# Kernel optimization log

Hardware: AMD Instinct MI355X
Metric: run time of the kernel (lower is better)

## Reference

```python
import jax, jax.numpy as jnp
import numpy as np

HIDDEN = 2048
NH = 32        # query heads
NKV = 4        # kv heads (GQA)
HD = 64        # head_dim
Q_SIZE = NH * HD      # 2048
KV_SIZE = NKV * HD    # 256
WINDOW = 1024         # sliding window size
THETA = 1000000.0
T = 2048              # tokens
SCALE = HD ** -0.5
NEG = -1e30


def setup_inputs() -> dict:
    key = jax.random.key(0)
    k1, k2, k3 = jax.random.split(key, 3)
    return {
        "positions": jnp.arange(T, dtype=jnp.int32),
        "hidden_states": jax.random.normal(k1, (T, HIDDEN), dtype=jnp.float32),
        "wqkv": jax.random.normal(k2, (HIDDEN, Q_SIZE + 2 * KV_SIZE), dtype=jnp.float32) * (HIDDEN ** -0.5),
        "wo": jax.random.normal(k3, (Q_SIZE, HIDDEN), dtype=jnp.float32) * (Q_SIZE ** -0.5),
    }


def _apply_rope(x, positions):
    # NeoX-style rotary embedding over full head_dim (rotate halves).
    half = HD // 2
    inv_freq = 1.0 / (THETA ** (jnp.arange(half, dtype=jnp.float32) / half))
    ang = positions.astype(jnp.float32)[:, None] * inv_freq[None, :]   # [T, half]
    cos = jnp.cos(ang)[:, None, :]   # [T, 1, half]
    sin = jnp.sin(ang)[:, None, :]
    x1, x2 = jnp.split(x, 2, axis=-1)
    return jnp.concatenate([x1 * cos - x2 * sin, x2 * cos + x1 * sin], axis=-1)


def reference(positions, hidden_states, wqkv, wo):
    # fused QKV projection
    qkv = hidden_states @ wqkv                          # [T, Q+2KV]
    q = qkv[:, :Q_SIZE].reshape(T, NH, HD)
    k = qkv[:, Q_SIZE:Q_SIZE + KV_SIZE].reshape(T, NKV, HD)
    v = qkv[:, Q_SIZE + KV_SIZE:].reshape(T, NKV, HD)
    # rotary embedding on q, k
    q = _apply_rope(q, positions)
    k = _apply_rope(k, positions)
    # GQA: repeat kv heads to match query heads
    group = NH // NKV
    kr = jnp.repeat(k, group, axis=1)                   # [T, NH, HD]
    vr = jnp.repeat(v, group, axis=1)
    scores = jnp.einsum('qhd,khd->hqk', q, kr) * SCALE  # [NH, T, T]
    # causal + sliding-window mask: attend to j in (i-WINDOW, i]
    i = jnp.arange(T)[:, None]
    j = jnp.arange(T)[None, :]
    mask = (j <= i) & (i - j < WINDOW)                  # [T, T]
    scores = jnp.where(mask[None, :, :], scores, NEG)
    probs = jax.nn.softmax(scores, axis=-1)
    attn = jnp.einsum('hqk,khd->qhd', probs, vr).reshape(T, Q_SIZE)
    return attn @ wo                                    # [T, HIDDEN]
```

## Files before the change

kernel.cpp:

```cpp
#include <hip/hip_runtime.h>
#include <hip/hip_bf16.h>

typedef float  f32x4  __attribute__((ext_vector_type(4)));
typedef __bf16 bf16x8 __attribute__((ext_vector_type(8)));
typedef __bf16 bf16x4 __attribute__((ext_vector_type(4)));
typedef __bf16 bf16x2 __attribute__((ext_vector_type(2)));

#define T_SEQ   2048
#define HIDDEN  2048
#define NH      32
#define NKV     4
#define HD      64
#define QSZ     2048
#define KVSZ    256
#define QKVN    2560
#define WINDOW  1024

#if __has_builtin(__builtin_amdgcn_exp2f)
#define EXPS(x) __builtin_amdgcn_exp2f(x)
#define QSCALE  0.1803368801111f
#else
#define EXPS(x) __expf(x)
#define QSCALE  0.125f
#endif

#define RAW_BARRIER()   asm volatile("s_barrier" ::: "memory")
#define WAITV(n)        asm volatile("s_waitcnt vmcnt(" #n ")" ::: "memory")

__device__ __forceinline__ void gll16(const __bf16* g, __bf16* l) {
    __builtin_amdgcn_global_load_lds(
        (const __attribute__((address_space(1))) void*)g,
        (__attribute__((address_space(3))) void*)l,
        16, 0, 0);
}

__global__ __launch_bounds__(256) void prep(const float4* __restrict__ hidden4,
                                            bf16x4* __restrict__ hidden_bf4,
                                            const float* __restrict__ wqkv,
                                            __bf16* __restrict__ wqkv_t,
                                            const int* __restrict__ pos,
                                            float2* __restrict__ ropetab) {
    __shared__ float tile[32][132];
    const int b = blockIdx.x;
    const int tid = threadIdx.x;

    if (b < 4096) {
        int id = b * 256 + tid;
        float4 v = hidden4[id];
        bf16x4 o;
        o[0] = (__bf16)v.x; o[1] = (__bf16)v.y; o[2] = (__bf16)v.z; o[3] = (__bf16)v.w;
        hidden_bf4[id] = o;
        return;
    }
    if (b < 4352) {
        int id = (b - 4096) * 256 + tid;
        int row = id >> 5, f = id & 31;
        float p = (float)pos[row];
        float ifr = exp2f((float)f * -0.62286151779138f);
        float sn, cs;
        sincosf(p * ifr, &sn, &cs);
        ropetab[id] = make_float2(cs, sn);
        return;
    }

    int t = b - 4352;
    const int bx = t % 20, by = t / 20;
    const int ri = by * 32, ci = bx * 128;
    const int r0 = tid >> 5;
    const int c4 = tid & 31;
    #pragma unroll
    for (int i = 0; i < 4; i++) {
        float4 v = *reinterpret_cast<const float4*>(
            &wqkv[(size_t)(ri + r0 + i * 8) * QKVN + ci + c4 * 4]);
        *reinterpret_cast<float4*>(&tile[r0 + i * 8][c4 * 4]) = v;
    }
    __syncthreads();
    const int c  = tid >> 3;
    const int rb = tid & 7;
    #pragma unroll
    for (int j = 0; j < 4; j++) {
        int cc = c + j * 32;
        bf16x4 pk;
        #pragma unroll
        for (int i = 0; i < 4; i++) pk[i] = (__bf16)tile[rb * 4 + i][cc];
        *reinterpret_cast<bf16x4*>(&wqkv_t[(size_t)(ci + cc) * HIDDEN + ri + rb * 4]) = pk;
    }
}


#define GEMM_PROLOGUE_COMMON(Aptr, Btptr, Kdim)                                 \
    const int tid = threadIdx.x;                                                \
    const int wid = tid >> 6;                                                   \
    const int l   = tid & 63;                                                   \
    const int lg  = l >> 4;                                                     \
    const int ll  = l & 15;                                                     \
    const int swl = ll & 7;                                                     \
    const int wm  = wid >> 1, wn = wid & 1;                                     \
    const int gx   = gridDim.x;                                                 \
    const int flat = blockIdx.y * gx + blockIdx.x;                              \
    const int nwg  = gx * gridDim.y;                                            \
    const int swz  = (flat & 7) * (nwg >> 3) + (flat >> 3);                     \
    const int bm   = (swz / gx) * 64;                                           \
    const int bn   = (swz % gx) * 128;                                          \
    const __bf16* Ab = (Aptr) + (size_t)bm * (Kdim);                            \
    const __bf16* Bb = (Btptr) + (size_t)bn * (Kdim);                           \
    f32x4 acc[2][4];                                                            \
    _Pragma("unroll")                                                           \
    for (int i = 0; i < 2; i++)                                                 \
        _Pragma("unroll")                                                       \
        for (int j = 0; j < 4; j++)                                             \
            acc[i][j] = (f32x4){0.f, 0.f, 0.f, 0.f};                            \
    const int srow = tid >> 3;                                                  \
    const int sseg0 = tid & 7;

#define GEMM_STAGE(buf, k0, Kdim)                                               \
    {                                                                           \
        _Pragma("unroll")                                                       \
        for (int c = 0; c < 2; c++) {                                           \
            int row  = c * 32 + srow;                                           \
            int sseg = sseg0 ^ (row & 7);                                       \
            gll16(Ab + (size_t)row * (Kdim) + (k0) + sseg * 8,                  \
                  &Asm[buf][(c * 256 + tid) * 8]);                              \
        }                                                                       \
        _Pragma("unroll")                                                       \
        for (int c = 0; c < 4; c++) {                                           \
            int row  = c * 32 + srow;                                           \
            int sseg = sseg0 ^ (row & 7);                                       \
            gll16(Bb + (size_t)row * (Kdim) + (k0) + sseg * 8,                  \
                  &Bsm[buf][(c * 256 + tid) * 8]);                              \
        }                                                                       \
    }

#define GEMM_COMPUTE(bufidx)                                                    \
    _Pragma("unroll")                                                           \
    for (int ss = 0; ss < 2; ss++) {                                            \
        bf16x8 af[2], bfr[4];                                                   \
        _Pragma("unroll")                                                       \
        for (int mi = 0; mi < 2; mi++) {                                        \
            int r = wm * 32 + mi * 16 + ll;                                     \
            int u = (ss * 4 + lg) ^ swl;                                        \
            af[mi] = *reinterpret_cast<const bf16x8*>(&Asm[bufidx][r * 64 + u * 8]); \
        }                                                                       \
        _Pragma("unroll")                                                       \
        for (int ni = 0; ni < 4; ni++) {                                        \
            int r = wn * 64 + ni * 16 + ll;                                     \
            int u = (ss * 4 + lg) ^ swl;                                        \
            bfr[ni] = *reinterpret_cast<const bf16x8*>(&Bsm[bufidx][r * 64 + u * 8]); \
        }                                                                       \
        _Pragma("unroll")                                                       \
        for (int mi = 0; mi < 2; mi++)                                          \
            _Pragma("unroll")                                                   \
            for (int ni = 0; ni < 4; ni++)                                      \
                acc[mi][ni] = __builtin_amdgcn_mfma_f32_16x16x32_bf16(          \
                    af[mi], bfr[ni], acc[mi][ni], 0, 0, 0);                     \
    }

#define GEMM_KLOOP2(Kdim)                                                       \
    GEMM_STAGE(0, 0, Kdim)                                                      \
    int cur = 0;                                                                \
    for (int k0 = 0; k0 < (Kdim); k0 += 64) {                                   \
        RAW_BARRIER();                                                          \
        if (k0 + 64 < (Kdim)) {                                                 \
            GEMM_STAGE(cur ^ 1, k0 + 64, Kdim)                                  \
            WAITV(6);                                                           \
        } else {                                                                \
            WAITV(0);                                                           \
        }                                                                       \
        RAW_BARRIER();                                                          \
        __builtin_amdgcn_sched_barrier(0);                                      \
        GEMM_COMPUTE(cur)                                                       \
        cur ^= 1;                                                               \
    }

#define GEMM_KLOOP3(Kdim)                                                       \
    GEMM_STAGE(0, 0, Kdim)                                                      \
    GEMM_STAGE(1, 64, Kdim)                                                     \
    int cur = 0;                                                                \
    for (int k0 = 0; k0 < (Kdim); k0 += 64) {                                   \
        if (k0 + 64 < (Kdim)) { WAITV(6); } else { WAITV(0); }                  \
        RAW_BARRIER();                                                          \
        __builtin_amdgcn_sched_barrier(0);                                      \
        if (k0 + 128 < (Kdim)) {                                                \
            int nb = cur + 2; if (nb >= 3) nb -= 3;                             \
            GEMM_STAGE(nb, k0 + 128, Kdim)                                      \
        }                                                                       \
        GEMM_COMPUTE(cur)                                                       \
        cur = (cur == 2) ? 0 : cur + 1;                                         \
    }

__global__ __launch_bounds__(256) void gemm_out(const __bf16* __restrict__ A,
                                                const __bf16* __restrict__ Bt,
                                                float* __restrict__ Cout,
                                                int M, int N, int K) {
    __shared__ __align__(16) __bf16 Asm[3][64 * 64];
    __shared__ __align__(16) __bf16 Bsm[3][128 * 64];
    GEMM_PROLOGUE_COMMON(A, Bt, K)
    GEMM_KLOOP3(K)
    #pragma unroll
    for (int mi = 0; mi < 2; mi++)
        #pragma unroll
        for (int ni = 0; ni < 4; ni++)
            #pragma unroll
            for (int r = 0; r < 4; r++) {
                int row = bm + wm*32 + mi*16 + lg*4 + r;
                int col = bn + wn*64 + ni*16 + ll;
                Cout[(size_t)row * N + col] = acc[mi][ni][r];
            }
}

__global__ __launch_bounds__(256) void gemm_qkv(const __bf16* __restrict__ A,
                                                const __bf16* __restrict__ Bt,
                                                const float2* __restrict__ ropetab,
                                                __bf16* __restrict__ q,
                                                __bf16* __restrict__ k,
                                                __bf16* __restrict__ vT) {
    __shared__ __align__(16) __bf16 Asm[2][64 * 64];
    __shared__ __align__(16) __bf16 Bsm[2][128 * 64];
    GEMM_PROLOGUE_COMMON(A, Bt, HIDDEN)
    GEMM_KLOOP2(HIDDEN)

    if (bn < QSZ + KVSZ) {
        const bool isq = (bn < QSZ);
        #pragma unroll
        for (int mi = 0; mi < 2; mi++) {
            #pragma unroll
            for (int r = 0; r < 4; r++) {
                int row = bm + wm*32 + mi*16 + lg*4 + r;
                const float2* tb = &ropetab[row * 32 + ll];
                #pragma unroll
                for (int ni = 0; ni < 2; ni++) {
                    float2 cssn = tb[ni * 16];
                    float x1 = acc[mi][ni][r], x2 = acc[mi][ni + 2][r];
                    float o1 = x1 * cssn.x - x2 * cssn.y;
                    float o2 = x2 * cssn.x + x1 * cssn.y;
                    int col = bn + wn*64 + ni*16 + ll;
                    if (isq) {
                        q[(size_t)row * QSZ + col]      = (__bf16)(o1 * QSCALE);
                        q[(size_t)row * QSZ + col + 32] = (__bf16)(o2 * QSCALE);
                    } else {
                        k[(size_t)row * KVSZ + (col - QSZ)]      = (__bf16)o1;
                        k[(size_t)row * KVSZ + (col - QSZ) + 32] = (__bf16)o2;
                    }
                }
            }
        }
    } else {
        #pragma unroll
        for (int mi = 0; mi < 2; mi++) {
            int row0 = bm + wm*32 + mi*16 + lg*4;
            #pragma unroll
            for (int ni = 0; ni < 4; ni++) {
                int d = bn + wn*64 + ni*16 + ll - (QSZ + KVSZ);
                bf16x4 pk;
                #pragma unroll
                for (int r = 0; r < 4; r++) pk[r] = (__bf16)acc[mi][ni][r];
                *reinterpret_cast<bf16x4*>(&vT[(size_t)d * T_SEQ + row0]) = pk;
            }
        }
    }
}

__global__ __launch_bounds__(512) void attn_fused(const __bf16* __restrict__ qg,
                                                  const __bf16* __restrict__ kgl,
                                                  const __bf16* __restrict__ vTg,
                                                  __bf16* __restrict__ og,
                                                  const float* __restrict__ wo,
                                                  __bf16* __restrict__ wo_t) {
    __shared__ __align__(16) char smem[49152];
    const int b   = blockIdx.x;
    const int tid = threadIdx.x;

    if (b >= 512) {
        float (*tile)[132] = (float(*)[132])smem;
        int t = b - 512;
        const int bx = t & 15, by = t >> 4;
        const int ri = by * 32, ci = bx * 128;
        const int r0 = tid >> 4;
        const int c8 = tid & 15;
        #pragma unroll
        for (int j = 0; j < 2; j++) {
            int col = c8 * 8 + j * 4;
            float4 v = *reinterpret_cast<const float4*>(
                &wo[(size_t)(ri + r0) * HIDDEN + ci + col]);
            *reinterpret_cast<float4*>(&tile[r0][col]) = v;
        }
        __syncthreads();
        #pragma unroll
        for (int j = 0; j < 2; j++) {
            int u  = tid + j * 512;
            int cc = u >> 3;
            int rb = u & 7;
            bf16x4 pk;
            #pragma unroll
            for (int i = 0; i < 4; i++) pk[i] = (__bf16)tile[rb * 4 + i][cc];
            *reinterpret_cast<bf16x4*>(&wo_t[(size_t)(ci + cc) * HIDDEN + ri + rb * 4]) = pk;
        }
        return;
    }

    __bf16* Ksm = (__bf16*)smem;
    __bf16* VTs = (__bf16*)(smem + 24576);
#define KSM(buf) (Ksm + (buf) * 4096)
#define VSM(buf) (VTs + (buf) * 4096)

    const int qb  = b & 31;
    const int hp  = b >> 5;
    const int kvh = hp >> 2;
    const int wid = tid >> 6;
    const int h   = hp * 2 + (wid >> 2);
    const int l   = tid & 63;
    const int lg  = l >> 4;
    const int ll  = l & 15;
    const int i0  = qb * 64;
    const int qw  = i0 + (wid & 3) * 16;
    const int qi  = qw + ll;

    bf16x8 qf[2];
    {
        const __bf16* qp = qg + (size_t)(qw + ll) * QSZ + h * 64 + lg * 8;
        qf[0] = *reinterpret_cast<const bf16x8*>(qp);
        qf[1] = *reinterpret_cast<const bf16x8*>(qp + 32);
    }

    f32x4 o[4];
    #pragma unroll
    for (int dn = 0; dn < 4; dn++) o[dn] = (f32x4){0.f, 0.f, 0.f, 0.f};
    float l_run = 0.f;

    int jlo = i0 - (WINDOW - 1); if (jlo < 0) jlo = 0;
    int t0v = jlo & ~63;
    int tend = i0 + 64;

    const int srow = tid >> 3;
    const int sg   = (tid & 7) ^ (srow & 7);
    const int krow = (srow & 35) | ((srow & 8) << 1) | ((srow & 4) << 1) | ((srow & 16) >> 2);
    const __bf16* kp = kgl + (size_t)krow * KVSZ + kvh * 64 + sg * 8;
    const __bf16* vp = vTg + (size_t)(kvh * 64 + srow) * T_SEQ + sg * 8;

#define ASTAGE(buf, t)                                   \
    {                                                    \
        gll16(kp + (size_t)(t) * KVSZ, KSM(buf) + tid * 8); \
        gll16(vp + (t),                VSM(buf) + tid * 8); \
    }

    ASTAGE(0, t0v);
    if (t0v + 64 < tend) ASTAGE(1, t0v + 64);

    const int swl = ll & 7;
    const int u0 = (lg ^ swl) * 8;
    const int u1 = ((4 + lg) ^ swl) * 8;

    int cur = 0;
    for (int t = t0v; t < tend; t += 64) {
        if (t + 64 < tend) { WAITV(2); } else { WAITV(0); }
        RAW_BARRIER();
        __builtin_amdgcn_sched_barrier(0);
        if (t + 128 < tend) {
            int nb = cur + 2; if (nb >= 3) nb -= 3;
            ASTAGE(nb, t + 128);
        }

        bool active = (t <= qw + 15) && (t + 63 >= qw - (WINDOW - 1));
        if (active) {
            f32x4 sT[4];
            __builtin_amdgcn_s_setprio(1);
            #pragma unroll
            for (int kt = 0; kt < 4; kt++) {
                sT[kt] = (f32x4){0.f, 0.f, 0.f, 0.f};
                bf16x8 kf0 = *reinterpret_cast<const bf16x8*>(KSM(cur) + kt*1024 + ll*64 + u0);
                sT[kt] = __builtin_amdgcn_mfma_f32_16x16x32_bf16(kf0, qf[0], sT[kt], 0, 0, 0);
                bf16x8 kf1 = *reinterpret_cast<const bf16x8*>(KSM(cur) + kt*1024 + ll*64 + u1);
                sT[kt] = __builtin_amdgcn_mfma_f32_16x16x32_bf16(kf1, qf[1], sT[kt], 0, 0, 0);
            }
            __builtin_amdgcn_s_setprio(0);

            bool full = (t + 63 <= qw) && (t >= qw + 15 - (WINDOW - 1));
            float ts = 0.f;
            if (full) {
                #pragma unroll
                for (int kt = 0; kt < 4; kt++) {
                    #pragma unroll
                    for (int r = 0; r < 4; r++) {
                        float p = EXPS(sT[kt][r]);
                        sT[kt][r] = p;
                        ts += p;
                    }
                }
            } else {
                #pragma unroll
                for (int kt = 0; kt < 4; kt++) {
                    int jb = t + ((kt & 2) << 4) + ((kt & 1) << 2) + (lg << 3);
                    #pragma unroll
                    for (int r = 0; r < 4; r++) {
                        int j = jb + r;
                        bool ok = (j <= qi) && (qi - j < WINDOW);
                        float p = ok ? EXPS(sT[kt][r]) : 0.f;
                        sT[kt][r] = p;
                        ts += p;
                    }
                }
            }
            ts += __shfl_xor(ts, 16);
            ts += __shfl_xor(ts, 32);
            l_run += ts;

            __builtin_amdgcn_s_setprio(1);
            #pragma unroll
            for (int kt2 = 0; kt2 < 2; kt2++) {
                bf16x8 pa;
                #pragma unroll
                for (int r = 0; r < 4; r++) {
                    pa[r]     = (__bf16)sT[kt2*2][r];
                    pa[r + 4] = (__bf16)sT[kt2*2 + 1][r];
                }
                int uv = kt2 ? u1 : u0;
                #pragma unroll
                for (int dn = 0; dn < 4; dn++) {
                    bf16x8 vf = *reinterpret_cast<const bf16x8*>(VSM(cur) + dn*1024 + ll*64 + uv);
                    o[dn] = __builtin_amdgcn_mfma_f32_16x16x32_bf16(pa, vf, o[dn], 0, 0, 0);
                }
            }
            __builtin_amdgcn_s_setprio(0);
        }
        cur = (cur == 2) ? 0 : cur + 1;
    }
#undef ASTAGE
#undef KSM
#undef VSM

    float linv = 1.0f / l_run;
    float i0v = __shfl(linv, lg*4 + 0);
    float i1v = __shfl(linv, lg*4 + 1);
    float i2v = __shfl(linv, lg*4 + 2);
    float i3v = __shfl(linv, lg*4 + 3);
    #pragma unroll
    for (int dn = 0; dn < 4; dn++) {
        og[(size_t)(qw + lg*4 + 0) * QSZ + h*64 + dn*16 + ll] = (__bf16)(o[dn][0] * i0v);
        og[(size_t)(qw + lg*4 + 1) * QSZ + h*64 + dn*16 + ll] = (__bf16)(o[dn][1] * i1v);
        og[(size_t)(qw + lg*4 + 2) * QSZ + h*64 + dn*16 + ll] = (__bf16)(o[dn][2] * i2v);
        og[(size_t)(qw + lg*4 + 3) * QSZ + h*64 + dn*16 + ll] = (__bf16)(o[dn][3] * i3v);
    }
}

extern "C" void kernel_launch(void* const* d_in, const int* in_sizes, int n_in,
                              void* d_out, int out_size, void* d_ws, size_t ws_size,
                              hipStream_t stream) {
    const int*   positions = (const int*)d_in[0];
    const float* hidden    = (const float*)d_in[1];
    const float* wqkv      = (const float*)d_in[2];
    const float* wo        = (const float*)d_in[3];
    float* out = (float*)d_out;

    char* ws = (char*)d_ws;
    __bf16* hidden_bf = (__bf16*)(ws);
    __bf16* wqkv_t    = (__bf16*)(ws + 8388608);
    __bf16* wo_t      = (__bf16*)(ws + 18874368);
    __bf16* q_bf      = (__bf16*)(ws + 37748736);
    __bf16* k_bf      = (__bf16*)(ws + 46137344);
    __bf16* vT_bf     = (__bf16*)(ws + 47185920);
    __bf16* attn_bf   = (__bf16*)(ws + 48234496);
    float2* ropetab   = (float2*)(ws + 56623104);

    prep<<<dim3(5632), dim3(256), 0, stream>>>(
        (const float4*)hidden, (bf16x4*)hidden_bf, wqkv, wqkv_t, positions, ropetab);

    gemm_qkv<<<dim3(QKVN / 128, T_SEQ / 64), dim3(256), 0, stream>>>(
        hidden_bf, wqkv_t, ropetab, q_bf, k_bf, vT_bf);

    attn_fused<<<dim3(1536), dim3(512), 0, stream>>>(
        q_bf, k_bf, vT_bf, attn_bf, wo, wo_t);

    gemm_out<<<dim3(HIDDEN / 128, T_SEQ / 64), dim3(256), 0, stream>>>(
        attn_bf, wo_t, out, T_SEQ, HIDDEN, QSZ);
}
```

Baseline: 102.0 us.

## Fuse fp32-to-bf16 hidden conversion into QKV GEMM A-tile loading

Removes the separate conversion pass that wrote a bf16 copy of hidden_states in prep. The QKV GEMM now loads fp32 A tiles into registers, converts them to bf16, and writes them to LDS, while B tiles still use direct global-to-LDS loads. This saves one full read and write of the activations plus a slice of the prep launch. In exchange, the GEMM reads twice the A bytes from global memory on every tile and now waits on register loads before the LDS writes, which may expose latency in the double-buffered loop.

```diff
diff --git a/kernel.cpp b/kernel.cpp
--- a/kernel.cpp
+++ b/kernel.cpp
@@ -26,6 +26,7 @@
 
 #define RAW_BARRIER()   asm volatile("s_barrier" ::: "memory")
 #define WAITV(n)        asm volatile("s_waitcnt vmcnt(" #n ")" ::: "memory")
+#define WAITLGKM0()     asm volatile("s_waitcnt lgkmcnt(0)" ::: "memory")
 
 __device__ __forceinline__ void gll16(const __bf16* g, __bf16* l) {
     __builtin_amdgcn_global_load_lds(
@@ -34,9 +35,7 @@
         16, 0, 0);
 }
 
-__global__ __launch_bounds__(256) void prep(const float4* __restrict__ hidden4,
-                                            bf16x4* __restrict__ hidden_bf4,
-                                            const float* __restrict__ wqkv,
+__global__ __launch_bounds__(256) void prep(const float* __restrict__ wqkv,
                                             __bf16* __restrict__ wqkv_t,
                                             const int* __restrict__ pos,
                                             float2* __restrict__ ropetab) {
@@ -44,16 +43,8 @@
     const int b = blockIdx.x;
     const int tid = threadIdx.x;
 
-    if (b < 4096) {
+    if (b < 256) {
         int id = b * 256 + tid;
-        float4 v = hidden4[id];
-        bf16x4 o;
-        o[0] = (__bf16)v.x; o[1] = (__bf16)v.y; o[2] = (__bf16)v.z; o[3] = (__bf16)v.w;
-        hidden_bf4[id] = o;
-        return;
-    }
-    if (b < 4352) {
-        int id = (b - 4096) * 256 + tid;
         int row = id >> 5, f = id & 31;
         float p = (float)pos[row];
         float ifr = exp2f((float)f * -0.62286151779138f);
@@ -63,7 +54,7 @@
         return;
     }
 
-    int t = b - 4352;
+    int t = b - 256;
     const int bx = t % 20, by = t / 20;
     const int ri = by * 32, ci = bx * 128;
     const int r0 = tid >> 5;
@@ -88,7 +79,7 @@
 }
 
 
-#define GEMM_PROLOGUE_COMMON(Aptr, Btptr, Kdim)                                 \
+#define GEMM_IDX_COMMON()                                                       \
     const int tid = threadIdx.x;                                                \
     const int wid = tid >> 6;                                                   \
     const int l   = tid & 63;                                                   \
@@ -102,8 +93,6 @@
     const int swz  = (flat & 7) * (nwg >> 3) + (flat >> 3);                     \
     const int bm   = (swz / gx) * 64;                                           \
     const int bn   = (swz % gx) * 128;                                          \
-    const __bf16* Ab = (Aptr) + (size_t)bm * (Kdim);                            \
-    const __bf16* Bb = (Btptr) + (size_t)bn * (Kdim);                           \
     f32x4 acc[2][4];                                                            \
     _Pragma("unroll")                                                           \
     for (int i = 0; i < 2; i++)                                                 \
@@ -155,23 +144,6 @@
                     af[mi], bfr[ni], acc[mi][ni], 0, 0, 0);                     \
     }
 
-#define GEMM_KLOOP2(Kdim)                                                       \
-    GEMM_STAGE(0, 0, Kdim)                                                      \
-    int cur = 0;                                                                \
-    for (int k0 = 0; k0 < (Kdim); k0 += 64) {                                   \
-        RAW_BARRIER();                                                          \
-        if (k0 + 64 < (Kdim)) {                                                 \
-            GEMM_STAGE(cur ^ 1, k0 + 64, Kdim)                                  \
-            WAITV(6);                                                           \
-        } else {                                                                \
-            WAITV(0);                                                           \
-        }                                                                       \
-        RAW_BARRIER();                                                          \
-        __builtin_amdgcn_sched_barrier(0);                                      \
-        GEMM_COMPUTE(cur)                                                       \
-        cur ^= 1;                                                               \
-    }
-
 #define GEMM_KLOOP3(Kdim)                                                       \
     GEMM_STAGE(0, 0, Kdim)                                                      \
     GEMM_STAGE(1, 64, Kdim)                                                     \
@@ -194,7 +166,9 @@
                                                 int M, int N, int K) {
     __shared__ __align__(16) __bf16 Asm[3][64 * 64];
     __shared__ __align__(16) __bf16 Bsm[3][128 * 64];
-    GEMM_PROLOGUE_COMMON(A, Bt, K)
+    GEMM_IDX_COMMON()
+    const __bf16* Ab = A  + (size_t)bm * K;
+    const __bf16* Bb = Bt + (size_t)bn * K;
     GEMM_KLOOP3(K)
     #pragma unroll
     for (int mi = 0; mi < 2; mi++)
@@ -208,7 +182,7 @@
             }
 }
 
-__global__ __launch_bounds__(256) void gemm_qkv(const __bf16* __restrict__ A,
+__global__ __launch_bounds__(256) void gemm_qkv(const float* __restrict__ Af,
                                                 const __bf16* __restrict__ Bt,
                                                 const float2* __restrict__ ropetab,
                                                 __bf16* __restrict__ q,
@@ -216,8 +190,68 @@
                                                 __bf16* __restrict__ vT) {
     __shared__ __align__(16) __bf16 Asm[2][64 * 64];
     __shared__ __align__(16) __bf16 Bsm[2][128 * 64];
-    GEMM_PROLOGUE_COMMON(A, Bt, HIDDEN)
-    GEMM_KLOOP2(HIDDEN)
+    GEMM_IDX_COMMON()
+    const float*  Ab = Af + (size_t)bm * HIDDEN;
+    const __bf16* Bb = Bt + (size_t)bn * HIDDEN;
+
+#define QKV_A_LOAD(k0)                                                          \
+    _Pragma("unroll")                                                           \
+    for (int c = 0; c < 2; c++) {                                               \
+        int row  = c * 32 + srow;                                               \
+        int useg = sseg0 ^ (row & 7);                                           \
+        const float4* src = reinterpret_cast<const float4*>(                    \
+            Ab + (size_t)row * HIDDEN + (k0) + useg * 8);                       \
+        fa[c][0] = src[0];                                                      \
+        fa[c][1] = src[1];                                                      \
+    }
+
+#define QKV_A_WRITE(buf)                                                        \
+    _Pragma("unroll")                                                           \
+    for (int c = 0; c < 2; c++) {                                               \
+        bf16x8 w;                                                               \
+        w[0] = (__bf16)fa[c][0].x; w[1] = (__bf16)fa[c][0].y;                   \
+        w[2] = (__bf16)fa[c][0].z; w[3] = (__bf16)fa[c][0].w;                   \
+        w[4] = (__bf16)fa[c][1].x; w[5] = (__bf16)fa[c][1].y;                   \
+        w[6] = (__bf16)fa[c][1].z; w[7] = (__bf16)fa[c][1].w;                   \
+        *reinterpret_cast<bf16x8*>(&Asm[buf][(c * 256 + tid) * 8]) = w;         \
+    }
+
+#define QKV_B_STAGE(buf, k0)                                                    \
+    _Pragma("unroll")                                                           \
+    for (int c = 0; c < 4; c++) {                                               \
+        int row  = c * 32 + srow;                                               \
+        int sseg = sseg0 ^ (row & 7);                                           \
+        gll16(Bb + (size_t)row * HIDDEN + (k0) + sseg * 8,                      \
+              &Bsm[buf][(c * 256 + tid) * 8]);                                  \
+    }
+
+    float4 fa[2][2];
+    QKV_A_LOAD(0)
+    QKV_B_STAGE(0, 0)
+    WAITV(4);
+    QKV_A_WRITE(0)
+
+    int cur = 0;
+    for (int k0 = 0; k0 < HIDDEN; k0 += 64) {
+        RAW_BARRIER();
+        if (k0 + 64 < HIDDEN) {
+            QKV_A_LOAD(k0 + 64)
+            QKV_B_STAGE(cur ^ 1, k0 + 64)
+            WAITV(4);
+            QKV_A_WRITE(cur ^ 1)
+            WAITLGKM0();
+        } else {
+            WAITV(0);
+            WAITLGKM0();
+        }
+        RAW_BARRIER();
+        __builtin_amdgcn_sched_barrier(0);
+        GEMM_COMPUTE(cur)
+        cur ^= 1;
+    }
+#undef QKV_A_LOAD
+#undef QKV_A_WRITE
+#undef QKV_B_STAGE
 
     if (bn < QSZ + KVSZ) {
         const bool isq = (bn < QSZ);
@@ -452,7 +486,6 @@
     float* out = (float*)d_out;
 
     char* ws = (char*)d_ws;
-    __bf16* hidden_bf = (__bf16*)(ws);
     __bf16* wqkv_t    = (__bf16*)(ws + 8388608);
     __bf16* wo_t      = (__bf16*)(ws + 18874368);
     __bf16* q_bf      = (__bf16*)(ws + 37748736);
@@ -461,11 +494,11 @@
     __bf16* attn_bf   = (__bf16*)(ws + 48234496);
     float2* ropetab   = (float2*)(ws + 56623104);
 
-    prep<<<dim3(5632), dim3(256), 0, stream>>>(
-        (const float4*)hidden, (bf16x4*)hidden_bf, wqkv, wqkv_t, positions, ropetab);
+    prep<<<dim3(1536), dim3(256), 0, stream>>>(
+        wqkv, wqkv_t, positions, ropetab);
 
     gemm_qkv<<<dim3(QKVN / 128, T_SEQ / 64), dim3(256), 0, stream>>>(
-        hidden_bf, wqkv_t, ropetab, q_bf, k_bf, vT_bf);
+        hidden, wqkv_t, ropetab, q_bf, k_bf, vT_bf);
 
     attn_fused<<<dim3(1536), dim3(512), 0, stream>>>(
         q_bf, k_bf, vT_bf, attn_bf, wo, wo_t);
```

Result: slower. 126.2 us (+23.8%).
